# Kernel optimization log

Hardware: AMD Instinct MI355X
Metric: run time of the kernel (lower is better)

## Reference

```python
import jax, jax.numpy as jnp
import numpy as np

N, IN_FEAT, OUT_FEAT = 16384, 1024, 4096


def setup_inputs() -> dict:
    key = jax.random.key(0)
    k_x, k_m, k_w, k_b = jax.random.split(key, 4)
    x = jax.random.normal(k_x, (N, IN_FEAT), dtype=jnp.float32)
    amask = jax.random.randint(k_m, (N,), 0, 2, dtype=jnp.int32)
    # nn.Linear(in_feat, out_feat): weight [out, in], bias [out]
    W = jax.random.normal(k_w, (OUT_FEAT, IN_FEAT), dtype=jnp.float32) * (1.0 / np.sqrt(IN_FEAT))
    b = jax.random.normal(k_b, (OUT_FEAT,), dtype=jnp.float32) * 0.001
    return {"x": x, "amask": amask, "W": W, "b": b}


def reference(x, amask, W, b):
    # Torch code gathers rows where amask != 0, applies linear (+identity act),
    # and scatters results back into a zero [N, out_feat] tensor. Equivalent
    # dense-math (jit-friendly, no data-dependent shapes): compute the linear
    # on all rows and zero out unmasked rows. Same output values.
    y = jnp.einsum('ni,oi->no', x, W) + b  # [N, out_feat]
    keep = (amask != 0)[:, None]
    return jnp.where(keep, y, jnp.zeros((), dtype=x.dtype))
```

## Files before the change

kernel.cpp:

```cpp
#include <hip/hip_runtime.h>
#include <hip/hip_bf16.h>
#include <stdint.h>

#define N_ROWS 16384
#define K_DIM  1024
#define N_OUT  4096

typedef __attribute__((ext_vector_type(8))) short short8;
typedef __attribute__((ext_vector_type(4))) float f32x4;
typedef __attribute__((ext_vector_type(4))) __bf16 bf16x4;

__global__ __launch_bounds__(1024) void prep_kernel(
    const int*   __restrict__ amask,
    const float* __restrict__ W,
    int* __restrict__ idx, int* __restrict__ zidx, int* __restrict__ count,
    __bf16* __restrict__ wb)
{
    const int t = threadIdx.x;
    if (blockIdx.x != 0) {
        const int i = (blockIdx.x - 1) * 1024 + t;
        float4 v = reinterpret_cast<const float4*>(W)[i];
        bf16x4 o;
        o[0] = (__bf16)v.x; o[1] = (__bf16)v.y; o[2] = (__bf16)v.z; o[3] = (__bf16)v.w;
        reinterpret_cast<bf16x4*>(wb)[i] = o;
        return;
    }
    __shared__ int sc[1024];
    const int base = t * 16;
    int mk[16];
#pragma unroll
    for (int g = 0; g < 4; ++g) {
        int4 m4 = reinterpret_cast<const int4*>(amask + base)[g];
        mk[g*4+0] = m4.x; mk[g*4+1] = m4.y; mk[g*4+2] = m4.z; mk[g*4+3] = m4.w;
    }
    int c = 0;
#pragma unroll
    for (int i = 0; i < 16; ++i) c += (mk[i] != 0) ? 1 : 0;
    int v = c;
    sc[t] = v;
    __syncthreads();
    for (int off = 1; off < 1024; off <<= 1) {
        int u = (t >= off) ? sc[t - off] : 0;
        __syncthreads();
        v += u; sc[t] = v;
        __syncthreads();
    }
    int b  = v - c;
    int zb = base - b;
#pragma unroll
    for (int i = 0; i < 16; ++i) {
        int r = base + i;
        if (mk[i] != 0) idx[b++] = r; else zidx[zb++] = r;
    }
    if (t == 1023) count[0] = v;
}

__global__ __launch_bounds__(256) void gather_zfill_kernel(
    const float* __restrict__ x, const int* __restrict__ idx,
    const int* __restrict__ zidx, const int* __restrict__ count,
    __bf16* __restrict__ xb, float* __restrict__ out) {
    const int t = threadIdx.x;
    if (blockIdx.x < 2048) {
        const int cnt = count[0];
        for (int j = blockIdx.x; j < cnt; j += 2048) {
            const int row = idx[j];
            float4 v = reinterpret_cast<const float4*>(x + (size_t)row * K_DIM)[t];
            bf16x4 o;
            o[0] = (__bf16)v.x; o[1] = (__bf16)v.y; o[2] = (__bf16)v.z; o[3] = (__bf16)v.w;
            reinterpret_cast<bf16x4*>(xb + (size_t)j * K_DIM)[t] = o;
        }
    } else {
        const int nz = N_ROWS - count[0];
        const int zb = blockIdx.x - 2048;
        const float4 zf = make_float4(0.f, 0.f, 0.f, 0.f);
        for (int i = zb; i < nz; i += 1024) {
            const int row = zidx[i];
            float4* p = reinterpret_cast<float4*>(out + (size_t)row * N_OUT);
#pragma unroll
            for (int u = 0; u < 4; ++u)
                p[u * 256 + t] = zf;
        }
    }
}


#define GLL(SRC, DSTOFF)                                                       \
    __builtin_amdgcn_global_load_lds(                                          \
        (const __attribute__((address_space(1))) void*)(SRC),                  \
        (__attribute__((address_space(3))) void*)(ldsc + (DSTOFF)), 16, 0, 0)

__global__ __launch_bounds__(256) void gemm_kernel(
    const __bf16* __restrict__ A,
    const __bf16* __restrict__ B,
    const float*  __restrict__ bias,
    const int*    __restrict__ idx,
    const int*    __restrict__ count,
    float*        __restrict__ out)
{
    __shared__ short lds_all[8192];

    const int cnt = count[0];
    const int aT  = (cnt + 127) >> 7;
    const int tn  = blockIdx.x & 31;
    const int tm  = blockIdx.x >> 5;
    if (tm >= aT) return;

    const int t  = threadIdx.x;
    const int l  = t & 63;
    const int w  = t >> 6;
    const int wm = w >> 1;
    const int wn = w & 1;

    const int m0 = tm * 128;
    const int n0 = tn * 128;

    const int srow = t >> 2;
    const int sk8  = (t & 3) * 8;
    const __bf16* pA0 = A + (size_t)(m0 + srow) * K_DIM + sk8;
    const __bf16* pA1 = pA0 + (size_t)64 * K_DIM;
    const __bf16* pB0 = B + (size_t)(n0 + srow) * K_DIM + sk8;
    const __bf16* pB1 = pB0 + (size_t)64 * K_DIM;
    char* ldsc = (char*)lds_all;

    const int lr = l & 15;
    const int lk = (l >> 4) * 8;

    f32x4 acc[4][4] = {};

    for (int k0 = 0; k0 < K_DIM; k0 += 32) {
        GLL(pA0 + k0, t * 16);
        GLL(pA1 + k0, 4096 + t * 16);
        GLL(pB0 + k0, 8192 + t * 16);
        GLL(pB1 + k0, 12288 + t * 16);
        __syncthreads();

        short8 af[4], bf[4];
#pragma unroll
        for (int mi = 0; mi < 4; ++mi)
            af[mi] = *(const short8*)(lds_all + (wm*64 + mi*16 + lr)*32 + lk);
#pragma unroll
        for (int ni = 0; ni < 4; ++ni)
            bf[ni] = *(const short8*)(lds_all + 4096 + (wn*64 + ni*16 + lr)*32 + lk);

#pragma unroll
        for (int mi = 0; mi < 4; ++mi)
#pragma unroll
            for (int ni = 0; ni < 4; ++ni)
                acc[mi][ni] = __builtin_amdgcn_mfma_f32_16x16x32_bf16(
                    af[mi], bf[ni], acc[mi][ni], 0, 0, 0);
        __syncthreads();
    }

    const int lq = l >> 4;
    float bv[4];
#pragma unroll
    for (int ni = 0; ni < 4; ++ni) bv[ni] = bias[n0 + wn*64 + ni*16 + lr];

#pragma unroll
    for (int mi = 0; mi < 4; ++mi) {
        const int slot0 = m0 + wm*64 + mi*16 + lq*4;
        int rowid[4]; bool val[4];
#pragma unroll
        for (int r = 0; r < 4; ++r) {
            const int s = slot0 + r;
            val[r] = (s < cnt);
            rowid[r] = val[r] ? idx[s] : 0;
        }
#pragma unroll
        for (int ni = 0; ni < 4; ++ni) {
            const int cc = n0 + wn*64 + ni*16 + lr;
#pragma unroll
            for (int r = 0; r < 4; ++r)
                if (val[r]) out[(size_t)rowid[r] * N_OUT + cc] = acc[mi][ni][r] + bv[ni];
        }
    }
}

__global__ void naive_kernel(const float* __restrict__ x, const float* __restrict__ W,
                             const float* __restrict__ bias, const int* __restrict__ amask,
                             float* __restrict__ out) {
    int c = blockIdx.x * blockDim.x + threadIdx.x;
    int r = blockIdx.y;
    if (c >= N_OUT) return;
    if (amask[r] == 0) { out[(size_t)r * N_OUT + c] = 0.0f; return; }
    const float* xr = x + (size_t)r * K_DIM;
    const float* wr = W + (size_t)c * K_DIM;
    float s = 0.0f;
    for (int k = 0; k < K_DIM; ++k) s += xr[k] * wr[k];
    out[(size_t)r * N_OUT + c] = s + bias[c];
}

extern "C" void kernel_launch(void* const* d_in, const int* in_sizes, int n_in,
                              void* d_out, int out_size, void* d_ws, size_t ws_size,
                              hipStream_t stream) {
    const float* x     = (const float*)d_in[0];
    const int*   amask = (const int*)d_in[1];
    const float* W     = (const float*)d_in[2];
    const float* bias  = (const float*)d_in[3];
    float*       out   = (float*)d_out;

    const size_t xb_bytes = (size_t)N_ROWS * K_DIM * 2;
    const size_t wb_bytes = (size_t)N_OUT  * K_DIM * 2;
    const size_t idx_bytes = (size_t)N_ROWS * 4;
    const size_t need = xb_bytes + wb_bytes + 2 * idx_bytes + 256;

    if (ws_size < need) {
        dim3 g((N_OUT + 255) / 256, N_ROWS);
        naive_kernel<<<g, 256, 0, stream>>>(x, W, bias, amask, out);
        return;
    }

    __bf16* xb   = (__bf16*)d_ws;
    __bf16* wb   = (__bf16*)((char*)d_ws + xb_bytes);
    int*    idx  = (int*)((char*)d_ws + xb_bytes + wb_bytes);
    int*    zidx = idx + N_ROWS;
    int*    cnt  = zidx + N_ROWS;

    prep_kernel<<<1025, 1024, 0, stream>>>(amask, W, idx, zidx, cnt, wb);
    gather_zfill_kernel<<<3072, 256, 0, stream>>>(x, idx, zidx, cnt, xb, out);
    gemm_kernel<<<4096, 256, 0, stream>>>(xb, wb, bias, idx, cnt, out);
}
```

Baseline: 154.8 us.

## Double GEMM K-step to 64, move zero-fill into idle GEMM blocks

The GEMM main loop now stages a 64-wide K slice per iteration (32 KB LDS), which halves the number of barrier pairs and runs two MFMA sub-steps per load. Zero-filling of unmasked output rows moves from the gather kernel into the GEMM blocks that have no work, so those blocks do useful stores instead of exiting. W conversion moves from the scan kernel into the gather kernel, leaving the scan as a single-block launch. The larger LDS footprint may lower occupancy, and the 128-byte LDS row stride may cause bank conflicts.

```diff
diff --git a/kernel.cpp b/kernel.cpp
--- a/kernel.cpp
+++ b/kernel.cpp
@@ -10,22 +10,12 @@
 typedef __attribute__((ext_vector_type(4))) float f32x4;
 typedef __attribute__((ext_vector_type(4))) __bf16 bf16x4;
 
-__global__ __launch_bounds__(1024) void prep_kernel(
-    const int*   __restrict__ amask,
-    const float* __restrict__ W,
-    int* __restrict__ idx, int* __restrict__ zidx, int* __restrict__ count,
-    __bf16* __restrict__ wb)
-{
+__global__ __launch_bounds__(1024) void scan_kernel(const int* __restrict__ amask,
+                                                    int* __restrict__ idx,
+                                                    int* __restrict__ zidx,
+                                                    int* __restrict__ count) {
+    __shared__ int sc[1024];
     const int t = threadIdx.x;
-    if (blockIdx.x != 0) {
-        const int i = (blockIdx.x - 1) * 1024 + t;
-        float4 v = reinterpret_cast<const float4*>(W)[i];
-        bf16x4 o;
-        o[0] = (__bf16)v.x; o[1] = (__bf16)v.y; o[2] = (__bf16)v.z; o[3] = (__bf16)v.w;
-        reinterpret_cast<bf16x4*>(wb)[i] = o;
-        return;
-    }
-    __shared__ int sc[1024];
     const int base = t * 16;
     int mk[16];
 #pragma unroll
@@ -55,31 +45,30 @@
     if (t == 1023) count[0] = v;
 }
 
-__global__ __launch_bounds__(256) void gather_zfill_kernel(
-    const float* __restrict__ x, const int* __restrict__ idx,
-    const int* __restrict__ zidx, const int* __restrict__ count,
-    __bf16* __restrict__ xb, float* __restrict__ out) {
+__global__ __launch_bounds__(256) void cvtw_gather_kernel(
+    const float* __restrict__ W, const float* __restrict__ x,
+    const int* __restrict__ idx, const int* __restrict__ count,
+    __bf16* __restrict__ wb, __bf16* __restrict__ xb) {
     const int t = threadIdx.x;
-    if (blockIdx.x < 2048) {
-        const int cnt = count[0];
-        for (int j = blockIdx.x; j < cnt; j += 2048) {
-            const int row = idx[j];
-            float4 v = reinterpret_cast<const float4*>(x + (size_t)row * K_DIM)[t];
+    if (blockIdx.x < 256) {
+        const int base = blockIdx.x * 4096 + t;
+#pragma unroll
+        for (int it = 0; it < 16; ++it) {
+            const int i = base + it * 256;
+            float4 v = reinterpret_cast<const float4*>(W)[i];
             bf16x4 o;
             o[0] = (__bf16)v.x; o[1] = (__bf16)v.y; o[2] = (__bf16)v.z; o[3] = (__bf16)v.w;
-            reinterpret_cast<bf16x4*>(xb + (size_t)j * K_DIM)[t] = o;
-        }
-    } else {
-        const int nz = N_ROWS - count[0];
-        const int zb = blockIdx.x - 2048;
-        const float4 zf = make_float4(0.f, 0.f, 0.f, 0.f);
-        for (int i = zb; i < nz; i += 1024) {
-            const int row = zidx[i];
-            float4* p = reinterpret_cast<float4*>(out + (size_t)row * N_OUT);
-#pragma unroll
-            for (int u = 0; u < 4; ++u)
-                p[u * 256 + t] = zf;
-        }
+            reinterpret_cast<bf16x4*>(wb)[i] = o;
+        }
+        return;
+    }
+    const int cnt = count[0];
+    for (int j = blockIdx.x - 256; j < cnt; j += 2048) {
+        const int row = idx[j];
+        float4 v = reinterpret_cast<const float4*>(x + (size_t)row * K_DIM)[t];
+        bf16x4 o;
+        o[0] = (__bf16)v.x; o[1] = (__bf16)v.y; o[2] = (__bf16)v.z; o[3] = (__bf16)v.w;
+        reinterpret_cast<bf16x4*>(xb + (size_t)j * K_DIM)[t] = o;
     }
 }
 
@@ -94,18 +83,33 @@
     const __bf16* __restrict__ B,
     const float*  __restrict__ bias,
     const int*    __restrict__ idx,
+    const int*    __restrict__ zidx,
     const int*    __restrict__ count,
     float*        __restrict__ out)
 {
-    __shared__ short lds_all[8192];
+    __shared__ short lds_all[16384];
 
     const int cnt = count[0];
     const int aT  = (cnt + 127) >> 7;
     const int tn  = blockIdx.x & 31;
     const int tm  = blockIdx.x >> 5;
-    if (tm >= aT) return;
-
-    const int t  = threadIdx.x;
+    const int t   = threadIdx.x;
+
+    if (tm >= aT) {
+        const int ntriv = 4096 - aT * 32;
+        const int tr    = blockIdx.x - aT * 32;
+        const int nz    = N_ROWS - cnt;
+        const float4 zf = make_float4(0.f, 0.f, 0.f, 0.f);
+        for (int i = tr; i < nz; i += ntriv) {
+            const int row = zidx[i];
+            float4* p = reinterpret_cast<float4*>(out + (size_t)row * N_OUT);
+#pragma unroll
+            for (int u = 0; u < 4; ++u)
+                p[u * 256 + t] = zf;
+        }
+        return;
+    }
+
     const int l  = t & 63;
     const int w  = t >> 6;
     const int wm = w >> 1;
@@ -114,40 +118,44 @@
     const int m0 = tm * 128;
     const int n0 = tn * 128;
 
-    const int srow = t >> 2;
-    const int sk8  = (t & 3) * 8;
-    const __bf16* pA0 = A + (size_t)(m0 + srow) * K_DIM + sk8;
-    const __bf16* pA1 = pA0 + (size_t)64 * K_DIM;
-    const __bf16* pB0 = B + (size_t)(n0 + srow) * K_DIM + sk8;
-    const __bf16* pB1 = pB0 + (size_t)64 * K_DIM;
+    const int srow = t >> 3;
+    const int sk   = (t & 7) * 8;
+    const __bf16* pA = A + (size_t)(m0 + srow) * K_DIM + sk;
+    const __bf16* pB = B + (size_t)(n0 + srow) * K_DIM + sk;
     char* ldsc = (char*)lds_all;
 
-    const int lr = l & 15;
-    const int lk = (l >> 4) * 8;
+    const int lr  = l & 15;
+    const int lqb = (l >> 4) * 16;
 
     f32x4 acc[4][4] = {};
 
-    for (int k0 = 0; k0 < K_DIM; k0 += 32) {
-        GLL(pA0 + k0, t * 16);
-        GLL(pA1 + k0, 4096 + t * 16);
-        GLL(pB0 + k0, 8192 + t * 16);
-        GLL(pB1 + k0, 12288 + t * 16);
-        __syncthreads();
-
-        short8 af[4], bf[4];
-#pragma unroll
-        for (int mi = 0; mi < 4; ++mi)
-            af[mi] = *(const short8*)(lds_all + (wm*64 + mi*16 + lr)*32 + lk);
-#pragma unroll
-        for (int ni = 0; ni < 4; ++ni)
-            bf[ni] = *(const short8*)(lds_all + 4096 + (wn*64 + ni*16 + lr)*32 + lk);
-
-#pragma unroll
-        for (int mi = 0; mi < 4; ++mi)
+    for (int k0 = 0; k0 < K_DIM; k0 += 64) {
+#pragma unroll
+        for (int p = 0; p < 4; ++p) {
+            GLL(pA + k0 + (size_t)(p * 32) * K_DIM, p * 4096 + t * 16);
+            GLL(pB + k0 + (size_t)(p * 32) * K_DIM, 16384 + p * 4096 + t * 16);
+        }
+        __syncthreads();
+
+#pragma unroll
+        for (int s = 0; s < 2; ++s) {
+            short8 af[4], bf[4];
+#pragma unroll
+            for (int mi = 0; mi < 4; ++mi)
+                af[mi] = *(const short8*)((char*)lds_all +
+                         (wm*64 + mi*16 + lr) * 128 + s * 64 + lqb);
 #pragma unroll
             for (int ni = 0; ni < 4; ++ni)
-                acc[mi][ni] = __builtin_amdgcn_mfma_f32_16x16x32_bf16(
-                    af[mi], bf[ni], acc[mi][ni], 0, 0, 0);
+                bf[ni] = *(const short8*)((char*)lds_all + 16384 +
+                         (wn*64 + ni*16 + lr) * 128 + s * 64 + lqb);
+
+#pragma unroll
+            for (int mi = 0; mi < 4; ++mi)
+#pragma unroll
+                for (int ni = 0; ni < 4; ++ni)
+                    acc[mi][ni] = __builtin_amdgcn_mfma_f32_16x16x32_bf16(
+                        af[mi], bf[ni], acc[mi][ni], 0, 0, 0);
+        }
         __syncthreads();
     }
 
@@ -216,7 +224,7 @@
     int*    zidx = idx + N_ROWS;
     int*    cnt  = zidx + N_ROWS;
 
-    prep_kernel<<<1025, 1024, 0, stream>>>(amask, W, idx, zidx, cnt, wb);
-    gather_zfill_kernel<<<3072, 256, 0, stream>>>(x, idx, zidx, cnt, xb, out);
-    gemm_kernel<<<4096, 256, 0, stream>>>(xb, wb, bias, idx, cnt, out);
-}
+    scan_kernel<<<1, 1024, 0, stream>>>(amask, idx, zidx, cnt);
+    cvtw_gather_kernel<<<2304, 256, 0, stream>>>(W, x, idx, cnt, wb, xb);
+    gemm_kernel<<<4096, 256, 0, stream>>>(xb, wb, bias, idx, zidx, cnt, out);
+}
```

Result: slower. 181.7 us (+17.3%).
